# Optimization experiments

Hardware: AMD Instinct MI355X
Metric: run time of the kernel (lower is better)

Reference implementation:

```python
import jax, jax.numpy as jnp
import numpy as np

N_NODES = 100000
N_EDGES = 1600000
F_IN = 48
F_HID = 64


def setup_inputs() -> dict:
    key = jax.random.key(0)
    k1, k2, k3, k4 = jax.random.split(key, 4)
    x = jax.random.normal(k1, (N_NODES, F_IN), dtype=jnp.float32)
    edge_index = jax.random.randint(k2, (2, N_EDGES), 0, N_NODES, dtype=jnp.int64)
    W1 = jax.random.normal(k3, (F_IN, F_HID), dtype=jnp.float32) * (1.0 / np.sqrt(F_IN))
    b1 = jnp.zeros((F_HID,), dtype=jnp.float32)
    W2 = jax.random.normal(k4, (F_HID, 2), dtype=jnp.float32) * (1.0 / np.sqrt(F_HID))
    b2 = jnp.zeros((2,), dtype=jnp.float32)
    return {"x": x, "edge_index": edge_index, "W1": W1, "b1": b1, "W2": W2, "b2": b2}


def _gcn_prep(edge_index, n_nodes):
    # PyG GCNConv default: add self-loops, symmetric normalization D^-1/2 (A+I) D^-1/2
    loops = jnp.arange(n_nodes, dtype=edge_index.dtype)
    src = jnp.concatenate([edge_index[0], loops])
    dst = jnp.concatenate([edge_index[1], loops])
    deg = jax.ops.segment_sum(jnp.ones_like(dst, dtype=jnp.float32), dst,
                              num_segments=n_nodes)
    dinv = jnp.where(deg > 0, jax.lax.rsqrt(deg), 0.0)
    norm = dinv[src] * dinv[dst]  # [E+N]
    return src, dst, norm


def _gcn_conv(h, W, b, src, dst, norm, n_nodes):
    h = h @ W                          # [N, F_out] linear first (PyG order)
    msg = h[src] * norm[:, None]       # gather + edge-scale
    agg = jax.ops.segment_sum(msg, dst, num_segments=n_nodes)  # scatter-add
    return agg + b


def reference(x, edge_index, W1, b1, W2, b2):
    n = x.shape[0]
    src, dst, norm = _gcn_prep(edge_index, n)
    h = jax.nn.relu(_gcn_conv(x, W1, b1, src, dst, norm, n))
    return _gcn_conv(h, W2, b2, src, dst, norm, n)
```

## Files before the change

kernel.cpp:

```cpp
#include <hip/hip_runtime.h>
#include <hip/hip_fp16.h>

#define F_IN 48
#define F_HID 64
#define GSH 7
#define GSZ 128
#define MAXB 1024
#define CAPSH 12
#define CAP 4096
#define CHUNK 4096

__device__ __forceinline__ bool detect64(const int* __restrict__ e) {
    return ((e[1] | e[3] | e[5] | e[7]) == 0);
}
__device__ __forceinline__ int load_src(const int* e, int i, int E, bool is64) {
    return e[is64 ? (long)2 * i : (long)i];
}
__device__ __forceinline__ int load_dst(const int* e, int i, int E, bool is64) {
    return e[is64 ? (long)2 * (E + i) : (long)(E + i)];
}
__device__ __forceinline__ float rdlane(float v, int l) {
    return __uint_as_float(__builtin_amdgcn_readlane(__float_as_uint(v), l));
}

__global__ __launch_bounds__(256) void passA(const int* __restrict__ e,
                                             int* __restrict__ bcnt,
                                             int* __restrict__ ebuf, int E, int B) {
    __shared__ int lcnt[MAXB], lbase[MAXB];
    bool is64 = detect64(e);
    bool vec = ((E & 3) == 0);
    int base = blockIdx.x * CHUNK;
    for (int t = threadIdx.x; t < B; t += 256) lcnt[t] = 0;
    __syncthreads();
    int pk[16], bk[16], rk[16];
#pragma unroll
    for (int g = 0; g < 4; ++g) {
        int i = base + (((g << 8) + (int)threadIdx.x) << 2);
        int r = g * 4;
        if (vec && i + 3 < E) {
            int4 s4, d4;
            if (is64) {
                const int4* p = (const int4*)(e + (size_t)2 * i);
                int4 a = p[0], bb = p[1];
                s4 = make_int4(a.x, a.z, bb.x, bb.z);
                const int4* q = (const int4*)(e + (size_t)2 * E + (size_t)2 * i);
                int4 c = q[0], dd = q[1];
                d4 = make_int4(c.x, c.z, dd.x, dd.z);
            } else {
                s4 = *(const int4*)(e + i);
                d4 = *(const int4*)(e + E + i);
            }
            int ss[4] = {s4.x, s4.y, s4.z, s4.w};
            int dv[4] = {d4.x, d4.y, d4.z, d4.w};
#pragma unroll
            for (int u = 0; u < 4; ++u) {
                pk[r + u] = ss[u] | ((dv[u] & (GSZ - 1)) << 17);
                bk[r + u] = dv[u] >> GSH;
                rk[r + u] = atomicAdd(&lcnt[bk[r + u]], 1);
            }
        } else {
#pragma unroll
            for (int u = 0; u < 4; ++u) {
                int ii = i + u;
                if (ii < E) {
                    int s = load_src(e, ii, E, is64);
                    int d = load_dst(e, ii, E, is64);
                    pk[r + u] = s | ((d & (GSZ - 1)) << 17);
                    bk[r + u] = d >> GSH;
                    rk[r + u] = atomicAdd(&lcnt[bk[r + u]], 1);
                } else {
                    bk[r + u] = -1;
                }
            }
        }
    }
    __syncthreads();
    for (int t = threadIdx.x; t < B; t += 256) {
        int c = lcnt[t];
        lbase[t] = c ? atomicAdd(&bcnt[t], c) : 0;
    }
    __syncthreads();
#pragma unroll
    for (int r = 0; r < 16; ++r) {
        if (bk[r] >= 0) {
            int pos = lbase[bk[r]] + rk[r];
            if (pos < CAP) ebuf[((size_t)bk[r] << CAPSH) + pos] = pk[r];
        }
    }
}

__global__ __launch_bounds__(256) void passB(const int* __restrict__ ebuf,
                                             const int* __restrict__ bcnt,
                                             const float* __restrict__ x,
                                             int* __restrict__ rowStart,
                                             int* __restrict__ deg,
                                             float* __restrict__ dinv,
                                             int* __restrict__ srcSorted,
                                             __half* __restrict__ y, int N) {
    __shared__ int cnt[GSZ], inc[GSZ], exo[GSZ];
    __shared__ float ldinv[GSZ];
    int b = blockIdx.x, t = threadIdx.x;
    int m = min(bcnt[b], CAP);
    const int* eb = ebuf + ((size_t)b << CAPSH);
    if (t < GSZ) cnt[t] = 0;
    __syncthreads();
    int gk[16], sk[16], rk[16];
    int iters = (m + 255) >> 8;
    for (int it = 0; it < iters; ++it) {
        int i = t + (it << 8);
        if (i < m) {
            int pkv = eb[i];
            gk[it] = pkv >> 17;
            sk[it] = pkv & 0x1FFFF;
            rk[it] = atomicAdd(&cnt[gk[it]], 1);
        } else {
            gk[it] = -1;
        }
    }
    __syncthreads();
    int myc = (t < GSZ) ? cnt[t] : 0;
    if (t < GSZ) inc[t] = myc;
    __syncthreads();
    for (int o = 1; o < GSZ; o <<= 1) {
        int v = (t < GSZ && t >= o) ? inc[t - o] : 0;
        __syncthreads();
        if (t < GSZ) inc[t] += v;
        __syncthreads();
    }
    if (t < GSZ) {
        int ex = inc[t] - myc;
        exo[t] = ex;
        float di = rsqrtf((float)myc + 1.0f);
        ldinv[t] = di;
        int node = (b << GSH) + t;
        if (node < N) {
            rowStart[node] = (b << CAPSH) + ex;
            deg[node] = myc;
            dinv[node] = di;
        }
    }
    __syncthreads();
    int s0b = b << CAPSH;
    for (int it = 0; it < iters; ++it) {
        if (gk[it] >= 0)
            srcSorted[s0b + exo[gk[it]] + rk[it]] = sk[it];
    }
    int nodeBase = b << GSH;
    for (int q = t; q < GSZ * 16; q += 256) {
        int nl = q >> 4, k4 = (q & 15) << 2;
        int node = nodeBase + nl;
        if (node < N) {
            ushort4 hv;
            if (k4 < F_IN) {
                float di = ldinv[nl];
                float4 xv = *(const float4*)(x + (size_t)node * F_IN + k4);
                hv.x = __half_as_ushort(__float2half(di * xv.x));
                hv.y = __half_as_ushort(__float2half(di * xv.y));
                hv.z = __half_as_ushort(__float2half(di * xv.z));
                hv.w = __half_as_ushort(__float2half(di * xv.w));
            } else {
                hv.x = hv.y = hv.z = hv.w = 0;
            }
            *(ushort4*)((char*)y + ((size_t)node << 7) + ((size_t)k4 << 1)) = hv;
        }
    }
}

__global__ __launch_bounds__(256) void fused1(const __half* __restrict__ y,
                                              const float* __restrict__ W1,
                                              const float* __restrict__ b1,
                                              const float* __restrict__ W2,
                                              const float* __restrict__ dinv,
                                              const int* __restrict__ rowStart,
                                              const int* __restrict__ deg,
                                              const int* __restrict__ srcSorted,
                                              float* __restrict__ g2, int N) {
    const int lane = threadIdx.x & 63;
    const int sub = lane >> 5;
    const int fl = lane & 31;
    const int base = blockIdx.x * 16 + (threadIdx.x >> 6) * 4;
    const char* yb = (const char*)y;
    const unsigned fb = (unsigned)fl << 2;

    int n0 = base, n1 = base + 1, n2 = base + 2, n3 = base + 3;
    int dn0 = (n0 < N) ? deg[n0] : -1;
    int dn1 = (n1 < N) ? deg[n1] : -1;
    int dn2_ = (n2 < N) ? deg[n2] : -1;
    int dn3 = (n3 < N) ? deg[n3] : -1;
    int rs0 = (n0 < N) ? rowStart[n0] : 0;
    int rs1 = (n1 < N) ? rowStart[n1] : 0;
    int rs2 = (n2 < N) ? rowStart[n2] : 0;
    int rs3 = (n3 < N) ? rowStart[n3] : 0;

    int idx0 = N, idx1 = N, idx2 = N, idx3 = N;
    if (lane < dn0) idx0 = srcSorted[rs0 + lane]; else if (lane == dn0) idx0 = n0;
    if (lane < dn1) idx1 = srcSorted[rs1 + lane]; else if (lane == dn1) idx1 = n1;
    if (lane < dn2_) idx2 = srcSorted[rs2 + lane]; else if (lane == dn2_) idx2 = n2;
    if (lane < dn3) idx3 = srcSorted[rs3 + lane]; else if (lane == dn3) idx3 = n3;

    float ax0 = 0, ay0 = 0, ax1 = 0, ay1 = 0;
    float ax2 = 0, ay2 = 0, ax3 = 0, ay3 = 0;

    auto step = [&](int p) {
        int sA = 2 * p + sub;
        unsigned o0 = ((unsigned)__shfl(idx0, sA, 64) << 7) + fb;
        unsigned o1 = ((unsigned)__shfl(idx1, sA, 64) << 7) + fb;
        unsigned o2 = ((unsigned)__shfl(idx2, sA, 64) << 7) + fb;
        unsigned o3 = ((unsigned)__shfl(idx3, sA, 64) << 7) + fb;
        float2 f0 = __half22float2(*(const __half2*)(yb + o0));
        float2 f1 = __half22float2(*(const __half2*)(yb + o1));
        float2 f2 = __half22float2(*(const __half2*)(yb + o2));
        float2 f3 = __half22float2(*(const __half2*)(yb + o3));
        ax0 += f0.x; ay0 += f0.y;
        ax1 += f1.x; ay1 += f1.y;
        ax2 += f2.x; ay2 += f2.y;
        ax3 += f3.x; ay3 += f3.y;
    };
#pragma unroll
    for (int p = 0; p < 12; ++p) step(p);
    int maxSlot = max(max(dn0, dn1), max(dn2_, dn3)) + 1;
    for (int p = 12; p < 32 && 2 * p < maxSlot; ++p) step(p);
    if (maxSlot > 64) {
        const __half2* yp = (const __half2*)y;
        for (int s = 64; s < maxSlot; ++s) {
            if (sub == 0) {
                if (s <= dn0) { float2 f = __half22float2(yp[((long)((s < dn0) ? srcSorted[rs0 + s] : n0) << 5) + fl]); ax0 += f.x; ay0 += f.y; }
                if (s <= dn1) { float2 f = __half22float2(yp[((long)((s < dn1) ? srcSorted[rs1 + s] : n1) << 5) + fl]); ax1 += f.x; ay1 += f.y; }
                if (s <= dn2_) { float2 f = __half22float2(yp[((long)((s < dn2_) ? srcSorted[rs2 + s] : n2) << 5) + fl]); ax2 += f.x; ay2 += f.y; }
                if (s <= dn3) { float2 f = __half22float2(yp[((long)((s < dn3) ? srcSorted[rs3 + s] : n3) << 5) + fl]); ax3 += f.x; ay3 += f.y; }
            }
        }
    }

    ax0 += __shfl(ax0, lane ^ 32, 64); ay0 += __shfl(ay0, lane ^ 32, 64);
    ax1 += __shfl(ax1, lane ^ 32, 64); ay1 += __shfl(ay1, lane ^ 32, 64);
    ax2 += __shfl(ax2, lane ^ 32, 64); ay2 += __shfl(ay2, lane ^ 32, 64);
    ax3 += __shfl(ax3, lane ^ 32, 64); ay3 += __shfl(ay3, lane ^ 32, 64);
    float di0 = (n0 < N) ? dinv[n0] : 0.0f;
    float di1 = (n1 < N) ? dinv[n1] : 0.0f;
    float di2 = (n2 < N) ? dinv[n2] : 0.0f;
    float di3 = (n3 < N) ? dinv[n3] : 0.0f;
    ax0 *= di0; ay0 *= di0; ax1 *= di1; ay1 *= di1;
    ax2 *= di2; ay2 *= di2; ax3 *= di3; ay3 *= di3;

    float h0 = b1[lane], h1 = h0, h2 = h0, h3 = h0;
#pragma unroll
    for (int k = 0; k < F_IN; k += 2) {
        float wA = W1[k * F_HID + lane];
        float wB = W1[(k + 1) * F_HID + lane];
        const int q = k >> 1;
        h0 = fmaf(rdlane(ax0, q), wA, h0); h0 = fmaf(rdlane(ay0, q), wB, h0);
        h1 = fmaf(rdlane(ax1, q), wA, h1); h1 = fmaf(rdlane(ay1, q), wB, h1);
        h2 = fmaf(rdlane(ax2, q), wA, h2); h2 = fmaf(rdlane(ay2, q), wB, h2);
        h3 = fmaf(rdlane(ax3, q), wA, h3); h3 = fmaf(rdlane(ay3, q), wB, h3);
    }
    h0 = fmaxf(h0, 0.0f); h1 = fmaxf(h1, 0.0f);
    h2 = fmaxf(h2, 0.0f); h3 = fmaxf(h3, 0.0f);

    float2 w2 = ((const float2*)W2)[lane];
    float t00 = h0 * w2.x, t01 = h0 * w2.y;
    float t10 = h1 * w2.x, t11 = h1 * w2.y;
    float t20 = h2 * w2.x, t21 = h2 * w2.y;
    float t30 = h3 * w2.x, t31 = h3 * w2.y;
#pragma unroll
    for (int off = 32; off > 0; off >>= 1) {
        t00 += __shfl_down(t00, off, 64); t01 += __shfl_down(t01, off, 64);
        t10 += __shfl_down(t10, off, 64); t11 += __shfl_down(t11, off, 64);
        t20 += __shfl_down(t20, off, 64); t21 += __shfl_down(t21, off, 64);
        t30 += __shfl_down(t30, off, 64); t31 += __shfl_down(t31, off, 64);
    }
    if (lane == 0) {
        float2* g2v = (float2*)g2;
        if (n0 < N) g2v[n0] = make_float2(di0 * t00, di0 * t01);
        if (n1 < N) g2v[n1] = make_float2(di1 * t10, di1 * t11);
        if (n2 < N) g2v[n2] = make_float2(di2 * t20, di2 * t21);
        if (n3 < N) g2v[n3] = make_float2(di3 * t30, di3 * t31);
    }
}

__global__ __launch_bounds__(256) void agg2(const int* __restrict__ rowStart,
                                            const int* __restrict__ deg,
                                            const int* __restrict__ srcSorted,
                                            const float* __restrict__ g2,
                                            const float* __restrict__ dinv,
                                            const float* __restrict__ b2,
                                            float* __restrict__ out, int N) {
    int gid = blockIdx.x * 256 + threadIdx.x;
    int node = gid >> 4, l16 = gid & 15;
    if (node >= N) return;
    const char* gb = (const char*)g2;
    int rs = rowStart[node], dn = deg[node];
    float a0 = 0.0f, a1 = 0.0f;
    for (int j = l16; j < dn; j += 16) {
        unsigned o = (unsigned)srcSorted[rs + j] << 3;
        float2 v = *(const float2*)(gb + o);
        a0 += v.x;
        a1 += v.y;
    }
#pragma unroll
    for (int m = 1; m < 16; m <<= 1) {
        a0 += __shfl_xor(a0, m, 64);
        a1 += __shfl_xor(a1, m, 64);
    }
    if (l16 == 0) {
        float2 self = *(const float2*)(gb + ((unsigned)node << 3));
        float di = dinv[node];
        out[2 * node + 0] = di * (a0 + self.x) + b2[0];
        out[2 * node + 1] = di * (a1 + self.y) + b2[1];
    }
}

extern "C" void kernel_launch(void* const* d_in, const int* in_sizes, int n_in,
                              void* d_out, int out_size, void* d_ws, size_t ws_size,
                              hipStream_t stream) {
    const float* x  = (const float*)d_in[0];
    const int* eidx = (const int*)d_in[1];
    const float* W1 = (const float*)d_in[2];
    const float* b1 = (const float*)d_in[3];
    const float* W2 = (const float*)d_in[4];
    const float* b2 = (const float*)d_in[5];
    float* out = (float*)d_out;

    int N = in_sizes[0] / F_IN;
    int E = in_sizes[1] / 2;
    int B = (N + GSZ - 1) >> GSH;

    char* ws = (char*)d_ws;
    __half* y16       = (__half*)ws;   ws += (size_t)(N + 1) * 64 * 2;
    int*    bcnt      = (int*)ws;      ws += MAXB * 4;
    int*    deg       = (int*)ws;      ws += (size_t)N * 4;
    int*    rowStart  = (int*)ws;      ws += (size_t)N * 4;
    float*  dinv      = (float*)ws;    ws += (size_t)N * 4;
    float*  g2        = (float*)ws;    ws += (size_t)N * 2 * 4;
    ws = (char*)(((size_t)ws + 255) & ~(size_t)255);
    int*    ebuf      = (int*)ws;      ws += (size_t)MAXB * CAP * 4;
    int*    srcSorted = (int*)ws;      ws += (size_t)MAXB * CAP * 4;

    hipMemsetAsync(y16 + (size_t)N * 64, 0, 128 + MAXB * 4, stream);

    passA<<<(E + CHUNK - 1) / CHUNK, 256, 0, stream>>>(eidx, bcnt, ebuf, E, B);
    passB<<<B, 256, 0, stream>>>(ebuf, bcnt, x, rowStart, deg, dinv, srcSorted,
                                 y16, N);
    fused1<<<(N + 15) / 16, 256, 0, stream>>>(y16, W1, b1, W2, dinv, rowStart, deg,
                                              srcSorted, g2, N);
    agg2<<<(N * 16 + 255) / 256, 256, 0, stream>>>(rowStart, deg, srcSorted, g2,
                                                   dinv, b2, out, N);
}
```

Baseline: 172.0 us.

## Pad CSR rows with self-loop and dummy slots, gather with scalar indices

```diff
diff --git a/kernel.cpp b/kernel.cpp
--- a/kernel.cpp
+++ b/kernel.cpp
@@ -8,7 +8,11 @@
 #define MAXB 1024
 #define CAPSH 12
 #define CAP 4096
+#define CAPE (CAP - GSZ)
+#define SSH 13
+#define SCAP 8192
 #define CHUNK 4096
+#define FIXS 24
 
 __device__ __forceinline__ bool detect64(const int* __restrict__ e) {
     return ((e[1] | e[3] | e[5] | e[7]) == 0);
@@ -21,6 +25,11 @@
 }
 __device__ __forceinline__ float rdlane(float v, int l) {
     return __uint_as_float(__builtin_amdgcn_readlane(__float_as_uint(v), l));
+}
+__device__ __forceinline__ void fmix2(float& alo, float& ahi, unsigned h) {
+    asm("v_fma_mix_f32 %0, %2, 1.0, %0 op_sel_hi:[1,0,0]\n\t"
+        "v_fma_mix_f32 %1, %2, 1.0, %1 op_sel:[1,0,0] op_sel_hi:[1,0,0]"
+        : "+v"(alo), "+v"(ahi) : "v"(h));
 }
 
 __global__ __launch_bounds__(256) void passA(const int* __restrict__ e,
@@ -84,7 +93,7 @@
     for (int r = 0; r < 16; ++r) {
         if (bk[r] >= 0) {
             int pos = lbase[bk[r]] + rk[r];
-            if (pos < CAP) ebuf[((size_t)bk[r] << CAPSH) + pos] = pk[r];
+            if (pos < CAPE) ebuf[((size_t)bk[r] << CAPSH) + pos] = pk[r];
         }
     }
 }
@@ -100,7 +109,7 @@
     __shared__ int cnt[GSZ], inc[GSZ], exo[GSZ];
     __shared__ float ldinv[GSZ];
     int b = blockIdx.x, t = threadIdx.x;
-    int m = min(bcnt[b], CAP);
+    int m = min(bcnt[b], CAPE);
     const int* eb = ebuf + ((size_t)b << CAPSH);
     if (t < GSZ) cnt[t] = 0;
     __syncthreads();
@@ -119,7 +128,8 @@
     }
     __syncthreads();
     int myc = (t < GSZ) ? cnt[t] : 0;
-    if (t < GSZ) inc[t] = myc;
+    int pl = (max(myc + 1, FIXS) + 1) & ~1;
+    if (t < GSZ) inc[t] = pl;
     __syncthreads();
     for (int o = 1; o < GSZ; o <<= 1) {
         int v = (t < GSZ && t >= o) ? inc[t - o] : 0;
@@ -128,19 +138,22 @@
         __syncthreads();
     }
     if (t < GSZ) {
-        int ex = inc[t] - myc;
+        int ex = inc[t] - pl;
         exo[t] = ex;
         float di = rsqrtf((float)myc + 1.0f);
         ldinv[t] = di;
         int node = (b << GSH) + t;
         if (node < N) {
-            rowStart[node] = (b << CAPSH) + ex;
+            rowStart[node] = (b << SSH) + ex;
             deg[node] = myc;
             dinv[node] = di;
         }
-    }
-    __syncthreads();
-    int s0b = b << CAPSH;
+        int* sb = srcSorted + ((size_t)b << SSH) + ex;
+        sb[myc] = node;
+        for (int j = myc + 1; j < pl; ++j) sb[j] = N;
+    }
+    __syncthreads();
+    int s0b = b << SSH;
     for (int it = 0; it < iters; ++it) {
         if (gk[it] >= 0)
             srcSorted[s0b + exo[gk[it]] + rk[it]] = sk[it];
@@ -176,66 +189,59 @@
                                               const int* __restrict__ srcSorted,
                                               float* __restrict__ g2, int N) {
     const int lane = threadIdx.x & 63;
-    const int sub = lane >> 5;
-    const int fl = lane & 31;
-    const int base = blockIdx.x * 16 + (threadIdx.x >> 6) * 4;
+    const int warp = __builtin_amdgcn_readfirstlane(threadIdx.x >> 6);
+    const int base = blockIdx.x * 16 + warp * 4;
     const char* yb = (const char*)y;
-    const unsigned fb = (unsigned)fl << 2;
+    const unsigned fb = (unsigned)(lane & 31) << 2;
 
     int n0 = base, n1 = base + 1, n2 = base + 2, n3 = base + 3;
-    int dn0 = (n0 < N) ? deg[n0] : -1;
-    int dn1 = (n1 < N) ? deg[n1] : -1;
-    int dn2_ = (n2 < N) ? deg[n2] : -1;
-    int dn3 = (n3 < N) ? deg[n3] : -1;
-    int rs0 = (n0 < N) ? rowStart[n0] : 0;
-    int rs1 = (n1 < N) ? rowStart[n1] : 0;
-    int rs2 = (n2 < N) ? rowStart[n2] : 0;
-    int rs3 = (n3 < N) ? rowStart[n3] : 0;
-
-    int idx0 = N, idx1 = N, idx2 = N, idx3 = N;
-    if (lane < dn0) idx0 = srcSorted[rs0 + lane]; else if (lane == dn0) idx0 = n0;
-    if (lane < dn1) idx1 = srcSorted[rs1 + lane]; else if (lane == dn1) idx1 = n1;
-    if (lane < dn2_) idx2 = srcSorted[rs2 + lane]; else if (lane == dn2_) idx2 = n2;
-    if (lane < dn3) idx3 = srcSorted[rs3 + lane]; else if (lane == dn3) idx3 = n3;
+    int dd0 = (n0 < N) ? __builtin_amdgcn_readfirstlane(deg[n0]) + 1 : 0;
+    int dd1 = (n1 < N) ? __builtin_amdgcn_readfirstlane(deg[n1]) + 1 : 0;
+    int dd2 = (n2 < N) ? __builtin_amdgcn_readfirstlane(deg[n2]) + 1 : 0;
+    int dd3 = (n3 < N) ? __builtin_amdgcn_readfirstlane(deg[n3]) + 1 : 0;
+    int rs0 = (n0 < N) ? __builtin_amdgcn_readfirstlane(rowStart[n0]) : 0;
+    int rs1 = (n1 < N) ? __builtin_amdgcn_readfirstlane(rowStart[n1]) : 0;
+    int rs2 = (n2 < N) ? __builtin_amdgcn_readfirstlane(rowStart[n2]) : 0;
+    int rs3 = (n3 < N) ? __builtin_amdgcn_readfirstlane(rowStart[n3]) : 0;
+    const int* sp0 = srcSorted + rs0;
+    const int* sp1 = srcSorted + rs1;
+    const int* sp2 = srcSorted + rs2;
+    const int* sp3 = srcSorted + rs3;
 
     float ax0 = 0, ay0 = 0, ax1 = 0, ay1 = 0;
     float ax2 = 0, ay2 = 0, ax3 = 0, ay3 = 0;
 
-    auto step = [&](int p) {
-        int sA = 2 * p + sub;
-        unsigned o0 = ((unsigned)__shfl(idx0, sA, 64) << 7) + fb;
-        unsigned o1 = ((unsigned)__shfl(idx1, sA, 64) << 7) + fb;
-        unsigned o2 = ((unsigned)__shfl(idx2, sA, 64) << 7) + fb;
-        unsigned o3 = ((unsigned)__shfl(idx3, sA, 64) << 7) + fb;
-        float2 f0 = __half22float2(*(const __half2*)(yb + o0));
-        float2 f1 = __half22float2(*(const __half2*)(yb + o1));
-        float2 f2 = __half22float2(*(const __half2*)(yb + o2));
-        float2 f3 = __half22float2(*(const __half2*)(yb + o3));
-        ax0 += f0.x; ay0 += f0.y;
-        ax1 += f1.x; ay1 += f1.y;
-        ax2 += f2.x; ay2 += f2.y;
-        ax3 += f3.x; ay3 += f3.y;
-    };
-#pragma unroll
-    for (int p = 0; p < 12; ++p) step(p);
-    int maxSlot = max(max(dn0, dn1), max(dn2_, dn3)) + 1;
-    for (int p = 12; p < 32 && 2 * p < maxSlot; ++p) step(p);
-    if (maxSlot > 64) {
-        const __half2* yp = (const __half2*)y;
-        for (int s = 64; s < maxSlot; ++s) {
-            if (sub == 0) {
-                if (s <= dn0) { float2 f = __half22float2(yp[((long)((s < dn0) ? srcSorted[rs0 + s] : n0) << 5) + fl]); ax0 += f.x; ay0 += f.y; }
-                if (s <= dn1) { float2 f = __half22float2(yp[((long)((s < dn1) ? srcSorted[rs1 + s] : n1) << 5) + fl]); ax1 += f.x; ay1 += f.y; }
-                if (s <= dn2_) { float2 f = __half22float2(yp[((long)((s < dn2_) ? srcSorted[rs2 + s] : n2) << 5) + fl]); ax2 += f.x; ay2 += f.y; }
-                if (s <= dn3) { float2 f = __half22float2(yp[((long)((s < dn3) ? srcSorted[rs3 + s] : n3) << 5) + fl]); ax3 += f.x; ay3 += f.y; }
-            }
-        }
-    }
-
-    ax0 += __shfl(ax0, lane ^ 32, 64); ay0 += __shfl(ay0, lane ^ 32, 64);
-    ax1 += __shfl(ax1, lane ^ 32, 64); ay1 += __shfl(ay1, lane ^ 32, 64);
-    ax2 += __shfl(ax2, lane ^ 32, 64); ay2 += __shfl(ay2, lane ^ 32, 64);
-    ax3 += __shfl(ax3, lane ^ 32, 64); ay3 += __shfl(ay3, lane ^ 32, 64);
+#pragma unroll
+    for (int s = 0; s < FIXS; ++s) {
+        unsigned i0 = (unsigned)__builtin_amdgcn_readfirstlane(sp0[s]);
+        unsigned i1 = (unsigned)__builtin_amdgcn_readfirstlane(sp1[s]);
+        unsigned i2 = (unsigned)__builtin_amdgcn_readfirstlane(sp2[s]);
+        unsigned i3 = (unsigned)__builtin_amdgcn_readfirstlane(sp3[s]);
+        unsigned v0 = *(const unsigned*)(yb + (((size_t)i0) << 7) + fb);
+        unsigned v1 = *(const unsigned*)(yb + (((size_t)i1) << 7) + fb);
+        unsigned v2 = *(const unsigned*)(yb + (((size_t)i2) << 7) + fb);
+        unsigned v3 = *(const unsigned*)(yb + (((size_t)i3) << 7) + fb);
+        fmix2(ax0, ay0, v0);
+        fmix2(ax1, ay1, v1);
+        fmix2(ax2, ay2, v2);
+        fmix2(ax3, ay3, v3);
+    }
+    int maxD = max(max(dd0, dd1), max(dd2, dd3));
+    for (int s = FIXS; s < maxD; ++s) {
+        unsigned i0 = (unsigned)((s < dd0) ? __builtin_amdgcn_readfirstlane(sp0[s]) : N);
+        unsigned i1 = (unsigned)((s < dd1) ? __builtin_amdgcn_readfirstlane(sp1[s]) : N);
+        unsigned i2 = (unsigned)((s < dd2) ? __builtin_amdgcn_readfirstlane(sp2[s]) : N);
+        unsigned i3 = (unsigned)((s < dd3) ? __builtin_amdgcn_readfirstlane(sp3[s]) : N);
+        unsigned v0 = *(const unsigned*)(yb + (((size_t)i0) << 7) + fb);
+        unsigned v1 = *(const unsigned*)(yb + (((size_t)i1) << 7) + fb);
+        unsigned v2 = *(const unsigned*)(yb + (((size_t)i2) << 7) + fb);
+        unsigned v3 = *(const unsigned*)(yb + (((size_t)i3) << 7) + fb);
+        fmix2(ax0, ay0, v0);
+        fmix2(ax1, ay1, v1);
+        fmix2(ax2, ay2, v2);
+        fmix2(ax3, ay3, v3);
+    }
+
     float di0 = (n0 < N) ? dinv[n0] : 0.0f;
     float di1 = (n1 < N) ? dinv[n1] : 0.0f;
     float di2 = (n2 < N) ? dinv[n2] : 0.0f;
@@ -289,9 +295,9 @@
     int node = gid >> 4, l16 = gid & 15;
     if (node >= N) return;
     const char* gb = (const char*)g2;
-    int rs = rowStart[node], dn = deg[node];
+    int rs = rowStart[node], dd = deg[node] + 1;
     float a0 = 0.0f, a1 = 0.0f;
-    for (int j = l16; j < dn; j += 16) {
+    for (int j = l16; j < dd; j += 16) {
         unsigned o = (unsigned)srcSorted[rs + j] << 3;
         float2 v = *(const float2*)(gb + o);
         a0 += v.x;
@@ -303,10 +309,9 @@
         a1 += __shfl_xor(a1, m, 64);
     }
     if (l16 == 0) {
-        float2 self = *(const float2*)(gb + ((unsigned)node << 3));
         float di = dinv[node];
-        out[2 * node + 0] = di * (a0 + self.x) + b2[0];
-        out[2 * node + 1] = di * (a1 + self.y) + b2[1];
+        out[2 * node + 0] = di * a0 + b2[0];
+        out[2 * node + 1] = di * a1 + b2[1];
     }
 }
 
@@ -334,7 +339,7 @@
     float*  g2        = (float*)ws;    ws += (size_t)N * 2 * 4;
     ws = (char*)(((size_t)ws + 255) & ~(size_t)255);
     int*    ebuf      = (int*)ws;      ws += (size_t)MAXB * CAP * 4;
-    int*    srcSorted = (int*)ws;      ws += (size_t)MAXB * CAP * 4;
+    int*    srcSorted = (int*)ws;      ws += (size_t)MAXB * SCAP * 4;
 
     hipMemsetAsync(y16 + (size_t)N * 64, 0, 128 + MAXB * 4, stream);
 
```

New measurement: 185.1 us. +7.6%, slower.

## Apply W1 before aggregation via separate GEMM kernel, batch gathers with fma_mix

Applied to the files above, without the earlier changes.

```diff
diff --git a/kernel.cpp b/kernel.cpp
--- a/kernel.cpp
+++ b/kernel.cpp
@@ -9,6 +9,7 @@
 #define CAPSH 12
 #define CAP 4096
 #define CHUNK 4096
+#define NPW 16
 
 __device__ __forceinline__ bool detect64(const int* __restrict__ e) {
     return ((e[1] | e[3] | e[5] | e[7]) == 0);
@@ -19,8 +20,10 @@
 __device__ __forceinline__ int load_dst(const int* e, int i, int E, bool is64) {
     return e[is64 ? (long)2 * (E + i) : (long)(E + i)];
 }
-__device__ __forceinline__ float rdlane(float v, int l) {
-    return __uint_as_float(__builtin_amdgcn_readlane(__float_as_uint(v), l));
+__device__ __forceinline__ void fmix2(float& alo, float& ahi, unsigned h) {
+    asm("v_fma_mix_f32 %0, %2, 1.0, %0 op_sel_hi:[1,0,0]\n\t"
+        "v_fma_mix_f32 %1, %2, 1.0, %1 op_sel:[1,0,0] op_sel_hi:[1,0,0]"
+        : "+v"(alo), "+v"(ahi) : "v"(h));
 }
 
 __global__ __launch_bounds__(256) void passA(const int* __restrict__ e,
@@ -91,14 +94,11 @@
 
 __global__ __launch_bounds__(256) void passB(const int* __restrict__ ebuf,
                                              const int* __restrict__ bcnt,
-                                             const float* __restrict__ x,
                                              int* __restrict__ rowStart,
                                              int* __restrict__ deg,
                                              float* __restrict__ dinv,
-                                             int* __restrict__ srcSorted,
-                                             __half* __restrict__ y, int N) {
+                                             int* __restrict__ srcSorted, int N) {
     __shared__ int cnt[GSZ], inc[GSZ], exo[GSZ];
-    __shared__ float ldinv[GSZ];
     int b = blockIdx.x, t = threadIdx.x;
     int m = min(bcnt[b], CAP);
     const int* eb = ebuf + ((size_t)b << CAPSH);
@@ -130,13 +130,11 @@
     if (t < GSZ) {
         int ex = inc[t] - myc;
         exo[t] = ex;
-        float di = rsqrtf((float)myc + 1.0f);
-        ldinv[t] = di;
         int node = (b << GSH) + t;
         if (node < N) {
             rowStart[node] = (b << CAPSH) + ex;
             deg[node] = myc;
-            dinv[node] = di;
+            dinv[node] = rsqrtf((float)myc + 1.0f);
         }
     }
     __syncthreads();
@@ -145,41 +143,49 @@
         if (gk[it] >= 0)
             srcSorted[s0b + exo[gk[it]] + rk[it]] = sk[it];
     }
-    int nodeBase = b << GSH;
-    for (int q = t; q < GSZ * 16; q += 256) {
-        int nl = q >> 4, k4 = (q & 15) << 2;
-        int node = nodeBase + nl;
-        if (node < N) {
-            ushort4 hv;
-            if (k4 < F_IN) {
-                float di = ldinv[nl];
-                float4 xv = *(const float4*)(x + (size_t)node * F_IN + k4);
-                hv.x = __half_as_ushort(__float2half(di * xv.x));
-                hv.y = __half_as_ushort(__float2half(di * xv.y));
-                hv.z = __half_as_ushort(__float2half(di * xv.z));
-                hv.w = __half_as_ushort(__float2half(di * xv.w));
-            } else {
-                hv.x = hv.y = hv.z = hv.w = 0;
-            }
-            *(ushort4*)((char*)y + ((size_t)node << 7) + ((size_t)k4 << 1)) = hv;
-        }
-    }
-}
-
-__global__ __launch_bounds__(256) void fused1(const __half* __restrict__ y,
-                                              const float* __restrict__ W1,
-                                              const float* __restrict__ b1,
-                                              const float* __restrict__ W2,
-                                              const float* __restrict__ dinv,
-                                              const int* __restrict__ rowStart,
-                                              const int* __restrict__ deg,
-                                              const int* __restrict__ srcSorted,
-                                              float* __restrict__ g2, int N) {
+}
+
+__global__ __launch_bounds__(256) void gemm1(const float* __restrict__ x,
+                                             const float* __restrict__ W1,
+                                             const float* __restrict__ dinv,
+                                             __half* __restrict__ H, int N) {
+    const int lane = threadIdx.x & 63;
+    const int warp = __builtin_amdgcn_readfirstlane((int)(threadIdx.x >> 6));
+    const int nb = (blockIdx.x * 4 + warp) * NPW;
+    float w[F_IN];
+#pragma unroll
+    for (int k = 0; k < F_IN; ++k) w[k] = W1[k * F_HID + lane];
+    for (int u = 0; u < NPW; u += 2) {
+        int na = nb + u, nb2 = nb + u + 1;
+        int nac = min(na, N - 1), nbc = min(nb2, N - 1);
+        const float* xra = x + (size_t)nac * F_IN;
+        const float* xrb = x + (size_t)nbc * F_IN;
+        float ha = 0.0f, hb = 0.0f;
+#pragma unroll
+        for (int k = 0; k < F_IN; ++k) {
+            ha = fmaf(xra[k], w[k], ha);
+            hb = fmaf(xrb[k], w[k], hb);
+        }
+        if (na < N)
+            H[(size_t)na * F_HID + lane] = __float2half(dinv[nac] * ha);
+        if (nb2 < N)
+            H[(size_t)nb2 * F_HID + lane] = __float2half(dinv[nbc] * hb);
+    }
+}
+
+__global__ __launch_bounds__(256) void agg1(const __half* __restrict__ H,
+                                            const float* __restrict__ b1,
+                                            const float* __restrict__ W2,
+                                            const float* __restrict__ dinv,
+                                            const int* __restrict__ rowStart,
+                                            const int* __restrict__ deg,
+                                            const int* __restrict__ srcSorted,
+                                            float* __restrict__ g2, int N) {
     const int lane = threadIdx.x & 63;
     const int sub = lane >> 5;
     const int fl = lane & 31;
     const int base = blockIdx.x * 16 + (threadIdx.x >> 6) * 4;
-    const char* yb = (const char*)y;
+    const char* hb = (const char*)H;
     const unsigned fb = (unsigned)fl << 2;
 
     int n0 = base, n1 = base + 1, n2 = base + 2, n3 = base + 3;
@@ -201,33 +207,59 @@
     float ax0 = 0, ay0 = 0, ax1 = 0, ay1 = 0;
     float ax2 = 0, ay2 = 0, ax3 = 0, ay3 = 0;
 
-    auto step = [&](int p) {
+    auto batch6 = [&](int p0) {
+        unsigned o[6][4], v[6][4];
+#pragma unroll
+        for (int p = 0; p < 6; ++p) {
+            int sA = 2 * (p0 + p) + sub;
+            o[p][0] = ((unsigned)__shfl(idx0, sA, 64) << 7) + fb;
+            o[p][1] = ((unsigned)__shfl(idx1, sA, 64) << 7) + fb;
+            o[p][2] = ((unsigned)__shfl(idx2, sA, 64) << 7) + fb;
+            o[p][3] = ((unsigned)__shfl(idx3, sA, 64) << 7) + fb;
+        }
+#pragma unroll
+        for (int p = 0; p < 6; ++p) {
+            v[p][0] = *(const unsigned*)(hb + o[p][0]);
+            v[p][1] = *(const unsigned*)(hb + o[p][1]);
+            v[p][2] = *(const unsigned*)(hb + o[p][2]);
+            v[p][3] = *(const unsigned*)(hb + o[p][3]);
+        }
+#pragma unroll
+        for (int p = 0; p < 6; ++p) {
+            fmix2(ax0, ay0, v[p][0]);
+            fmix2(ax1, ay1, v[p][1]);
+            fmix2(ax2, ay2, v[p][2]);
+            fmix2(ax3, ay3, v[p][3]);
+        }
+    };
+    batch6(0);
+    batch6(6);
+
+    int maxD = max(max(dn0, dn1), max(dn2_, dn3));
+    int maxSlot = maxD + 1;
+    for (int p = 12; p < 32 && 2 * p < maxSlot; ++p) {
         int sA = 2 * p + sub;
         unsigned o0 = ((unsigned)__shfl(idx0, sA, 64) << 7) + fb;
         unsigned o1 = ((unsigned)__shfl(idx1, sA, 64) << 7) + fb;
         unsigned o2 = ((unsigned)__shfl(idx2, sA, 64) << 7) + fb;
         unsigned o3 = ((unsigned)__shfl(idx3, sA, 64) << 7) + fb;
-        float2 f0 = __half22float2(*(const __half2*)(yb + o0));
-        float2 f1 = __half22float2(*(const __half2*)(yb + o1));
-        float2 f2 = __half22float2(*(const __half2*)(yb + o2));
-        float2 f3 = __half22float2(*(const __half2*)(yb + o3));
-        ax0 += f0.x; ay0 += f0.y;
-        ax1 += f1.x; ay1 += f1.y;
-        ax2 += f2.x; ay2 += f2.y;
-        ax3 += f3.x; ay3 += f3.y;
-    };
-#pragma unroll
-    for (int p = 0; p < 12; ++p) step(p);
-    int maxSlot = max(max(dn0, dn1), max(dn2_, dn3)) + 1;
-    for (int p = 12; p < 32 && 2 * p < maxSlot; ++p) step(p);
+        unsigned v0 = *(const unsigned*)(hb + o0);
+        unsigned v1 = *(const unsigned*)(hb + o1);
+        unsigned v2 = *(const unsigned*)(hb + o2);
+        unsigned v3 = *(const unsigned*)(hb + o3);
+        fmix2(ax0, ay0, v0);
+        fmix2(ax1, ay1, v1);
+        fmix2(ax2, ay2, v2);
+        fmix2(ax3, ay3, v3);
+    }
     if (maxSlot > 64) {
-        const __half2* yp = (const __half2*)y;
+        const __half2* hp = (const __half2*)H;
         for (int s = 64; s < maxSlot; ++s) {
             if (sub == 0) {
-                if (s <= dn0) { float2 f = __half22float2(yp[((long)((s < dn0) ? srcSorted[rs0 + s] : n0) << 5) + fl]); ax0 += f.x; ay0 += f.y; }
-                if (s <= dn1) { float2 f = __half22float2(yp[((long)((s < dn1) ? srcSorted[rs1 + s] : n1) << 5) + fl]); ax1 += f.x; ay1 += f.y; }
-                if (s <= dn2_) { float2 f = __half22float2(yp[((long)((s < dn2_) ? srcSorted[rs2 + s] : n2) << 5) + fl]); ax2 += f.x; ay2 += f.y; }
-                if (s <= dn3) { float2 f = __half22float2(yp[((long)((s < dn3) ? srcSorted[rs3 + s] : n3) << 5) + fl]); ax3 += f.x; ay3 += f.y; }
+                if (s <= dn0) { float2 f = __half22float2(hp[((long)((s < dn0) ? srcSorted[rs0 + s] : n0) << 5) + fl]); ax0 += f.x; ay0 += f.y; }
+                if (s <= dn1) { float2 f = __half22float2(hp[((long)((s < dn1) ? srcSorted[rs1 + s] : n1) << 5) + fl]); ax1 += f.x; ay1 += f.y; }
+                if (s <= dn2_) { float2 f = __half22float2(hp[((long)((s < dn2_) ? srcSorted[rs2 + s] : n2) << 5) + fl]); ax2 += f.x; ay2 += f.y; }
+                if (s <= dn3) { float2 f = __half22float2(hp[((long)((s < dn3) ? srcSorted[rs3 + s] : n3) << 5) + fl]); ax3 += f.x; ay3 += f.y; }
             }
         }
     }
@@ -240,34 +272,24 @@
     float di1 = (n1 < N) ? dinv[n1] : 0.0f;
     float di2 = (n2 < N) ? dinv[n2] : 0.0f;
     float di3 = (n3 < N) ? dinv[n3] : 0.0f;
-    ax0 *= di0; ay0 *= di0; ax1 *= di1; ay1 *= di1;
-    ax2 *= di2; ay2 *= di2; ax3 *= di3; ay3 *= di3;
-
-    float h0 = b1[lane], h1 = h0, h2 = h0, h3 = h0;
-#pragma unroll
-    for (int k = 0; k < F_IN; k += 2) {
-        float wA = W1[k * F_HID + lane];
-        float wB = W1[(k + 1) * F_HID + lane];
-        const int q = k >> 1;
-        h0 = fmaf(rdlane(ax0, q), wA, h0); h0 = fmaf(rdlane(ay0, q), wB, h0);
-        h1 = fmaf(rdlane(ax1, q), wA, h1); h1 = fmaf(rdlane(ay1, q), wB, h1);
-        h2 = fmaf(rdlane(ax2, q), wA, h2); h2 = fmaf(rdlane(ay2, q), wB, h2);
-        h3 = fmaf(rdlane(ax3, q), wA, h3); h3 = fmaf(rdlane(ay3, q), wB, h3);
-    }
-    h0 = fmaxf(h0, 0.0f); h1 = fmaxf(h1, 0.0f);
-    h2 = fmaxf(h2, 0.0f); h3 = fmaxf(h3, 0.0f);
-
-    float2 w2 = ((const float2*)W2)[lane];
-    float t00 = h0 * w2.x, t01 = h0 * w2.y;
-    float t10 = h1 * w2.x, t11 = h1 * w2.y;
-    float t20 = h2 * w2.x, t21 = h2 * w2.y;
-    float t30 = h3 * w2.x, t31 = h3 * w2.y;
-#pragma unroll
-    for (int off = 32; off > 0; off >>= 1) {
-        t00 += __shfl_down(t00, off, 64); t01 += __shfl_down(t01, off, 64);
-        t10 += __shfl_down(t10, off, 64); t11 += __shfl_down(t11, off, 64);
-        t20 += __shfl_down(t20, off, 64); t21 += __shfl_down(t21, off, 64);
-        t30 += __shfl_down(t30, off, 64); t31 += __shfl_down(t31, off, 64);
+
+    float2 b1v = *(const float2*)(b1 + 2 * fl);
+    float4 w2q = *(const float4*)(W2 + 4 * fl);
+    float hA, hB;
+    hA = fmaxf(fmaf(di0, ax0, b1v.x), 0.0f); hB = fmaxf(fmaf(di0, ay0, b1v.y), 0.0f);
+    float t00 = hA * w2q.x + hB * w2q.z, t01 = hA * w2q.y + hB * w2q.w;
+    hA = fmaxf(fmaf(di1, ax1, b1v.x), 0.0f); hB = fmaxf(fmaf(di1, ay1, b1v.y), 0.0f);
+    float t10 = hA * w2q.x + hB * w2q.z, t11 = hA * w2q.y + hB * w2q.w;
+    hA = fmaxf(fmaf(di2, ax2, b1v.x), 0.0f); hB = fmaxf(fmaf(di2, ay2, b1v.y), 0.0f);
+    float t20 = hA * w2q.x + hB * w2q.z, t21 = hA * w2q.y + hB * w2q.w;
+    hA = fmaxf(fmaf(di3, ax3, b1v.x), 0.0f); hB = fmaxf(fmaf(di3, ay3, b1v.y), 0.0f);
+    float t30 = hA * w2q.x + hB * w2q.z, t31 = hA * w2q.y + hB * w2q.w;
+#pragma unroll
+    for (int m = 1; m <= 16; m <<= 1) {
+        t00 += __shfl_xor(t00, m, 64); t01 += __shfl_xor(t01, m, 64);
+        t10 += __shfl_xor(t10, m, 64); t11 += __shfl_xor(t11, m, 64);
+        t20 += __shfl_xor(t20, m, 64); t21 += __shfl_xor(t21, m, 64);
+        t30 += __shfl_xor(t30, m, 64); t31 += __shfl_xor(t31, m, 64);
     }
     if (lane == 0) {
         float2* g2v = (float2*)g2;
@@ -326,7 +348,7 @@
     int B = (N + GSZ - 1) >> GSH;
 
     char* ws = (char*)d_ws;
-    __half* y16       = (__half*)ws;   ws += (size_t)(N + 1) * 64 * 2;
+    __half* H         = (__half*)ws;   ws += (size_t)(N + 1) * F_HID * 2;
     int*    bcnt      = (int*)ws;      ws += MAXB * 4;
     int*    deg       = (int*)ws;      ws += (size_t)N * 4;
     int*    rowStart  = (int*)ws;      ws += (size_t)N * 4;
@@ -336,13 +358,13 @@
     int*    ebuf      = (int*)ws;      ws += (size_t)MAXB * CAP * 4;
     int*    srcSorted = (int*)ws;      ws += (size_t)MAXB * CAP * 4;
 
-    hipMemsetAsync(y16 + (size_t)N * 64, 0, 128 + MAXB * 4, stream);
+    hipMemsetAsync(H + (size_t)N * F_HID, 0, 128 + MAXB * 4, stream);
 
     passA<<<(E + CHUNK - 1) / CHUNK, 256, 0, stream>>>(eidx, bcnt, ebuf, E, B);
-    passB<<<B, 256, 0, stream>>>(ebuf, bcnt, x, rowStart, deg, dinv, srcSorted,
-                                 y16, N);
-    fused1<<<(N + 15) / 16, 256, 0, stream>>>(y16, W1, b1, W2, dinv, rowStart, deg,
-                                              srcSorted, g2, N);
+    passB<<<B, 256, 0, stream>>>(ebuf, bcnt, rowStart, deg, dinv, srcSorted, N);
+    gemm1<<<(N + 4 * NPW - 1) / (4 * NPW), 256, 0, stream>>>(x, W1, dinv, H, N);
+    agg1<<<(N + 15) / 16, 256, 0, stream>>>(H, b1, W2, dinv, rowStart, deg,
+                                            srcSorted, g2, N);
     agg2<<<(N * 16 + 255) / 256, 256, 0, stream>>>(rowStart, deg, srcSorted, g2,
                                                    dinv, b2, out, N);
 }
```

New measurement: 178.5 us. 3.8% more time.

## Make edge bucketing two-pass per block with larger chunks

Applied to the files above, without the earlier changes.

```diff
diff --git a/kernel.cpp b/kernel.cpp
--- a/kernel.cpp
+++ b/kernel.cpp
@@ -8,7 +8,7 @@
 #define MAXB 1024
 #define CAPSH 12
 #define CAP 4096
-#define CHUNK 4096
+#define CHUNK 16384
 
 __device__ __forceinline__ bool detect64(const int* __restrict__ e) {
     return ((e[1] | e[3] | e[5] | e[7]) == 0);
@@ -30,13 +30,43 @@
     bool is64 = detect64(e);
     bool vec = ((E & 3) == 0);
     int base = blockIdx.x * CHUNK;
-    for (int t = threadIdx.x; t < B; t += 256) lcnt[t] = 0;
-    __syncthreads();
-    int pk[16], bk[16], rk[16];
-#pragma unroll
-    for (int g = 0; g < 4; ++g) {
+    for (int t = threadIdx.x; t < MAXB; t += 256) lcnt[t] = 0;
+    __syncthreads();
+    for (int g = 0; g < 16; ++g) {
         int i = base + (((g << 8) + (int)threadIdx.x) << 2);
-        int r = g * 4;
+        if (vec && i + 3 < E) {
+            int4 d4;
+            if (is64) {
+                const int4* q = (const int4*)(e + (size_t)2 * E + (size_t)2 * i);
+                int4 c = q[0], dd = q[1];
+                d4 = make_int4(c.x, c.z, dd.x, dd.z);
+            } else {
+                d4 = *(const int4*)(e + E + i);
+            }
+            atomicAdd(&lcnt[d4.x >> GSH], 1);
+            atomicAdd(&lcnt[d4.y >> GSH], 1);
+            atomicAdd(&lcnt[d4.z >> GSH], 1);
+            atomicAdd(&lcnt[d4.w >> GSH], 1);
+        } else {
+#pragma unroll
+            for (int u = 0; u < 4; ++u) {
+                int ii = i + u;
+                if (ii < E) {
+                    int d = load_dst(e, ii, E, is64);
+                    atomicAdd(&lcnt[d >> GSH], 1);
+                }
+            }
+        }
+    }
+    __syncthreads();
+    for (int t = threadIdx.x; t < B; t += 256) {
+        int c = lcnt[t];
+        lbase[t] = c ? atomicAdd(&bcnt[t], c) : 0;
+        lcnt[t] = 0;
+    }
+    __syncthreads();
+    for (int g = 0; g < 16; ++g) {
+        int i = base + (((g << 8) + (int)threadIdx.x) << 2);
         if (vec && i + 3 < E) {
             int4 s4, d4;
             if (is64) {
@@ -54,9 +84,11 @@
             int dv[4] = {d4.x, d4.y, d4.z, d4.w};
 #pragma unroll
             for (int u = 0; u < 4; ++u) {
-                pk[r + u] = ss[u] | ((dv[u] & (GSZ - 1)) << 17);
-                bk[r + u] = dv[u] >> GSH;
-                rk[r + u] = atomicAdd(&lcnt[bk[r + u]], 1);
+                int bk = dv[u] >> GSH;
+                int pos = lbase[bk] + atomicAdd(&lcnt[bk], 1);
+                if (pos < CAP)
+                    ebuf[((size_t)bk << CAPSH) + pos] =
+                        ss[u] | ((dv[u] & (GSZ - 1)) << 17);
             }
         } else {
 #pragma unroll
@@ -65,26 +97,13 @@
                 if (ii < E) {
                     int s = load_src(e, ii, E, is64);
                     int d = load_dst(e, ii, E, is64);
-                    pk[r + u] = s | ((d & (GSZ - 1)) << 17);
-                    bk[r + u] = d >> GSH;
-                    rk[r + u] = atomicAdd(&lcnt[bk[r + u]], 1);
-                } else {
-                    bk[r + u] = -1;
+                    int bk = d >> GSH;
+                    int pos = lbase[bk] + atomicAdd(&lcnt[bk], 1);
+                    if (pos < CAP)
+                        ebuf[((size_t)bk << CAPSH) + pos] =
+                            s | ((d & (GSZ - 1)) << 17);
                 }
             }
-        }
-    }
-    __syncthreads();
-    for (int t = threadIdx.x; t < B; t += 256) {
-        int c = lcnt[t];
-        lbase[t] = c ? atomicAdd(&bcnt[t], c) : 0;
-    }
-    __syncthreads();
-#pragma unroll
-    for (int r = 0; r < 16; ++r) {
-        if (bk[r] >= 0) {
-            int pos = lbase[bk[r]] + rk[r];
-            if (pos < CAP) ebuf[((size_t)bk[r] << CAPSH) + pos] = pk[r];
         }
     }
 }
```

After: 179.8 us. +4.5%, slower.
